# Optimization experiments

Measured on AMD Instinct MI355X. Metric: run time of the kernel, lower is better.

## Reference

```python
import jax, jax.numpy as jnp
import numpy as np

H = 16  # num_heads


def _rotate_half(t):
    d = t.shape[-1] // 2
    return jnp.concatenate((-t[..., d:], t[..., :d]), axis=-1)


def setup_inputs() -> dict:
    key = jax.random.key(0)
    ks = jax.random.split(key, 4)
    S, HID = 2048, 1280
    D = HID // H  # 80
    x = jax.random.normal(ks[0], (S, HID), dtype=jnp.float32)
    # rotary tables (seq_len, head_dim)
    inv_freq = 1.0 / (10000.0 ** (jnp.arange(0, D, 2, dtype=jnp.float32) / D))
    freqs = jnp.arange(S, dtype=jnp.float32)[:, None] * inv_freq[None, :]  # (S, D/2)
    emb = jnp.concatenate([freqs, freqs], axis=-1)  # (S, D)
    cos = jnp.cos(emb)
    sin = jnp.sin(emb)
    W_qkv = jax.random.normal(ks[1], (HID, 3 * HID), dtype=jnp.float32) * 0.02
    b_qkv = jnp.zeros((3 * HID,), dtype=jnp.float32)
    W_out = jax.random.normal(ks[2], (HID, HID), dtype=jnp.float32) * 0.02
    b_out = jnp.zeros((HID,), dtype=jnp.float32)
    # 8 windows of 256 tokens each -> block-diagonal attention
    cu_seqlens = jnp.arange(0, S + 1, 256, dtype=jnp.int32)  # (9,)
    return {"x": x, "cos": cos, "sin": sin, "W_qkv": W_qkv, "b_qkv": b_qkv,
            "W_out": W_out, "b_out": b_out, "cu_seqlens": cu_seqlens}


def _segment_mask(cu_seqlens, seq_len, dtype):
    positions = jnp.arange(seq_len)
    starts = cu_seqlens[:-1]
    ends = cu_seqlens[1:]
    in_segment = (positions[:, None] >= starts[None, :]) & (positions[:, None] < ends[None, :])
    segment_ids = jnp.argmax(in_segment.astype(jnp.int32), axis=-1)  # (S,)
    same_segment = segment_ids[:, None] == segment_ids[None, :]      # (S, S)
    return jnp.where(same_segment, jnp.zeros((), dtype), jnp.finfo(dtype).min)


def reference(x, cos, sin, W_qkv, b_qkv, W_out, b_out, cu_seqlens):
    S, HID = x.shape
    D = HID // H
    scale = D ** -0.5
    qkv = x @ W_qkv + b_qkv                       # (S, 3*HID)
    q, k, v = jnp.split(qkv, 3, axis=-1)
    q = q.reshape(S, H, D)
    k = k.reshape(S, H, D)
    v = v.reshape(S, H, D)
    cos_f = cos[:, :D][:, None, :]                # (S, 1, D)
    sin_f = sin[:, :D][:, None, :]
    q = q * cos_f + _rotate_half(q) * sin_f       # inline RoPE (fp32)
    k = k * cos_f + _rotate_half(k) * sin_f
    q = jnp.transpose(q, (1, 0, 2))               # (H, S, D)
    k = jnp.transpose(k, (1, 0, 2))
    v = jnp.transpose(v, (1, 0, 2))
    scores = jnp.einsum('hqd,hkd->hqk', q, k) * scale  # (H, S, S)
    mask = _segment_mask(cu_seqlens, S, scores.dtype)  # (S, S) block-diagonal bias
    scores = scores + mask[None, :, :]
    weights = jax.nn.softmax(scores, axis=-1)
    out = jnp.einsum('hqk,hkd->hqd', weights, v)       # (H, S, D)
    out = jnp.transpose(out, (1, 0, 2)).reshape(S, HID)
    return out @ W_out + b_out
```

## Files before the change

### kernel.cpp

```cpp
#include <hip/hip_runtime.h>


typedef short s16x8 __attribute__((ext_vector_type(8)));
typedef __bf16 bf16x8 __attribute__((ext_vector_type(8)));
typedef float f32x4 __attribute__((ext_vector_type(4)));
typedef unsigned short u16;
typedef unsigned long long u64;

__device__ __forceinline__ f32x4 mfma16(s16x8 a, s16x8 b, f32x4 c) {
  return __builtin_amdgcn_mfma_f32_16x16x32_bf16(
      __builtin_bit_cast(bf16x8, a), __builtin_bit_cast(bf16x8, b), c, 0, 0, 0);
}
__device__ __forceinline__ u16 f2b(float f) {
  union { float f; unsigned u; } v;
  v.f = f;
  unsigned r = v.u + 0x7fffu + ((v.u >> 16) & 1u);
  return (u16)(r >> 16);
}
__device__ __forceinline__ void gl16(const u16* g, u16* l) {
  __builtin_amdgcn_global_load_lds(
      (const __attribute__((address_space(1))) unsigned int*)(const void*)g,
      (__attribute__((address_space(3))) unsigned int*)(void*)l, 16, 0, 0);
}

__device__ __forceinline__ void transpose_body(const float* __restrict__ W,
                                               u16* __restrict__ WT, int K, int N,
                                               int nb, int kb, int t, float (*tile)[33]) {
  int tx = t & 31, ty = t >> 5;
#pragma unroll
  for (int r = 0; r < 32; r += 8)
    tile[ty + r][tx] = W[(long)(kb + ty + r) * N + nb + tx];
  __syncthreads();
#pragma unroll
  for (int r = 0; r < 32; r += 8)
    WT[(long)(nb + ty + r) * K + kb + tx] = f2b(tile[tx][ty + r]);
}

__global__ __launch_bounds__(256) void prep(const float* __restrict__ x,
                                            u16* __restrict__ xb,
                                            const float* __restrict__ Wqkv,
                                            u16* __restrict__ WqkvT,
                                            const float* __restrict__ Wout,
                                            u16* __restrict__ WoutT) {
  __shared__ float tile[32][33];
  int bid = blockIdx.x, t = threadIdx.x;
  if (bid < 2560) {
    int i = bid * 256 + t;
    float4 v = ((const float4*)x)[i];
    u64 pk = (u64)f2b(v.x) | ((u64)f2b(v.y) << 16) | ((u64)f2b(v.z) << 32) |
             ((u64)f2b(v.w) << 48);
    ((u64*)xb)[i] = pk;
  } else if (bid < 7360) {
    int i = bid - 2560;
    transpose_body(Wqkv, WqkvT, 1280, 3840, (i % 120) * 32, (i / 120) * 32, t, tile);
  } else {
    int i = bid - 7360;
    transpose_body(Wout, WoutT, 1280, 1280, (i % 40) * 32, (i / 40) * 32, t, tile);
  }
}

__global__ __launch_bounds__(256) void gemm_qkv_rope(const u16* __restrict__ A,
                                                     const u16* __restrict__ B,
                                                     const float* __restrict__ bias,
                                                     const float* __restrict__ cosb,
                                                     const float* __restrict__ sinb,
                                                     u16* __restrict__ Qr,
                                                     u16* __restrict__ Kr,
                                                     u16* __restrict__ VT) {
  __shared__ u16 As[64 * 32];
  __shared__ u16 Bs[160 * 32];
  const int K = 1280;
  int n0 = blockIdx.x * 160, m0 = blockIdx.y * 64;
  int t = threadIdx.x, w = t >> 6, lane = t & 63, lm = lane & 15, quad = lane >> 4;
  int wm = (w >> 1) * 32, wn = (w & 1) * 80;
  int srow = t >> 2;
  int scol = (((t & 3) ^ ((t >> 3) & 3))) * 8;
  const u16* Ag = A + (long)(m0 + srow) * K + scol;
  const u16* Bg = B + (long)(n0 + srow) * K + scol;
  const u16* Bg3 = B + (long)(n0 + 128 + srow) * K + scol;
  u16* AsW = As + w * 512;
  u16* BsW = Bs + w * 512;
  u16* BsW2 = Bs + 2048 + w * 512;
  u16* BsW3 = Bs + 4096 + w * 512;
  f32x4 acc[2][5] = {};
  for (int k0 = 0; k0 < K; k0 += 32) {
    __syncthreads();
    gl16(Ag + k0, AsW);
    gl16(Bg + k0, BsW);
    gl16(Bg + (long)64 * K + k0, BsW2);
    if (t < 128) gl16(Bg3 + k0, BsW3);
    __syncthreads();
    s16x8 af[2], bfr[5];
#pragma unroll
    for (int mt = 0; mt < 2; mt++) {
      int rm = wm + mt * 16 + lm;
      af[mt] = *(const s16x8*)&As[rm * 32 + ((quad ^ ((rm >> 1) & 3)) << 3)];
    }
#pragma unroll
    for (int nt = 0; nt < 5; nt++) {
      int rn = wn + nt * 16 + lm;
      bfr[nt] = *(const s16x8*)&Bs[rn * 32 + ((quad ^ ((rn >> 1) & 3)) << 3)];
    }
#pragma unroll
    for (int mt = 0; mt < 2; mt++)
#pragma unroll
      for (int nt = 0; nt < 5; nt++)
        acc[mt][nt] = mfma16(af[mt], bfr[nt], acc[mt][nt]);
  }

  int region = n0 / 1280;
  int hcol = (n0 - region * 1280 + wn) / 80;
  float bv[5];
#pragma unroll
  for (int nt = 0; nt < 5; nt++) bv[nt] = bias[n0 + wn + nt * 16 + lm];

  if (region == 2) {
#pragma unroll
    for (int mt = 0; mt < 2; mt++) {
      int sbase = m0 + wm + mt * 16 + quad * 4;
#pragma unroll
      for (int nt = 0; nt < 5; nt++) {
        int d = nt * 16 + lm;
        u64 pk = 0;
#pragma unroll
        for (int r = 0; r < 4; r++)
          pk |= (u64)f2b(acc[mt][nt][r] + bv[nt]) << (16 * r);
        *(u64*)&VT[((long)hcol * 80 + d) * 2048 + sbase] = pk;
      }
    }
    return;
  }

  const float scale = 0.111803398874989f;
  bool lo = lm < 8;
  u16* Out = (region == 0) ? Qr : Kr;
  float oscale = (region == 0) ? scale : 1.0f;
#pragma unroll
  for (int mt = 0; mt < 2; mt++)
#pragma unroll
    for (int r = 0; r < 4; r++) {
      int s = m0 + wm + mt * 16 + quad * 4 + r;
      float val[5], sw[5];
#pragma unroll
      for (int nt = 0; nt < 5; nt++) val[nt] = acc[mt][nt][r] + bv[nt];
#pragma unroll
      for (int nt = 0; nt < 5; nt++) sw[nt] = __shfl_xor(val[nt], 8);
      float rot[5];
      rot[0] = -(lo ? sw[2] : sw[3]);
      rot[1] = -(lo ? sw[3] : sw[4]);
      rot[2] = lo ? -sw[4] : sw[0];
      rot[3] = lo ? sw[0] : sw[1];
      rot[4] = lo ? sw[1] : sw[2];
      u16* orow = Out + ((long)hcol * 2048 + s) * 80;
      const float* crow = cosb + s * 80;
      const float* srw = sinb + s * 80;
#pragma unroll
      for (int nt = 0; nt < 5; nt++) {
        int d = nt * 16 + lm;
        orow[d] = f2b((val[nt] * crow[d] + rot[nt] * srw[d]) * oscale);
      }
    }
}

template <bool OUT_F32>
__global__ __launch_bounds__(256) void gemm_bt(const u16* __restrict__ A,
                                               const u16* __restrict__ B,
                                               const float* __restrict__ bias,
                                               void* __restrict__ Cout,
                                               int M, int N, int K) {
  __shared__ u16 As[64 * 32];
  __shared__ u16 Bs[128 * 32];
  int m0 = blockIdx.y * 64, n0 = blockIdx.x * 128;
  int t = threadIdx.x;
  int w = t >> 6, lane = t & 63, lm = lane & 15, quad = lane >> 4;
  int wm = (w >> 1) * 32, wn = (w & 1) * 64;
  int srow = t >> 2;
  int scol = (((t & 3) ^ ((t >> 3) & 3))) * 8;
  const u16* Ag = A + (long)(m0 + srow) * K + scol;
  const u16* Bg = B + (long)(n0 + srow) * K + scol;
  u16* AsW = As + w * 512;
  u16* BsW = Bs + w * 512;
  u16* BsW2 = Bs + 2048 + w * 512;
  f32x4 acc[2][4] = {};
  for (int k0 = 0; k0 < K; k0 += 32) {
    __syncthreads();
    gl16(Ag + k0, AsW);
    gl16(Bg + k0, BsW);
    gl16(Bg + (long)64 * K + k0, BsW2);
    __syncthreads();
    s16x8 af[2], bf[4];
#pragma unroll
    for (int mt = 0; mt < 2; mt++) {
      int rm = wm + mt * 16 + lm;
      af[mt] = *(const s16x8*)&As[rm * 32 + ((quad ^ ((rm >> 1) & 3)) << 3)];
    }
#pragma unroll
    for (int nt = 0; nt < 4; nt++) {
      int rn = wn + nt * 16 + lm;
      bf[nt] = *(const s16x8*)&Bs[rn * 32 + ((quad ^ ((rn >> 1) & 3)) << 3)];
    }
#pragma unroll
    for (int mt = 0; mt < 2; mt++)
#pragma unroll
      for (int nt = 0; nt < 4; nt++)
        acc[mt][nt] = mfma16(af[mt], bf[nt], acc[mt][nt]);
  }
#pragma unroll
  for (int mt = 0; mt < 2; mt++)
#pragma unroll
    for (int nt = 0; nt < 4; nt++) {
      int col = n0 + wn + nt * 16 + lm;
      float bvv = bias[col];
#pragma unroll
      for (int r = 0; r < 4; r++) {
        int row = m0 + wm + mt * 16 + quad * 4 + r;
        float v = acc[mt][nt][r] + bvv;
        if (OUT_F32) ((float*)Cout)[(long)row * N + col] = v;
        else ((u16*)Cout)[(long)row * N + col] = f2b(v);
      }
    }
}

__global__ __launch_bounds__(256, 1) void attn_kernel(const u16* __restrict__ Qr,
                                                      const u16* __restrict__ Kr,
                                                      const u16* __restrict__ VT,
                                                      u16* __restrict__ AO) {
  int qh = blockIdx.x, seg = blockIdx.y, h = blockIdx.z;
  int t = threadIdx.x;
  int w = t >> 6, lane = t & 63, lm = lane & 15, quad = lane >> 4;
  __shared__ u16 Ps[4][32 * 256];

  int s0 = seg * 256 + qh * 128 + w * 32;
  const u16* Qh = Qr + ((long)h * 2048 + s0) * 80;
  const u16* Kh = Kr + ((long)h * 2048 + seg * 256) * 80;

  f32x4 sc[2][16] = {};
  s16x8 zz = {};
#pragma unroll
  for (int kk = 0; kk < 3; kk++) {
    int dbase = kk * 32 + quad * 8;
    bool valid = dbase < 80;
    s16x8 af[2];
#pragma unroll
    for (int mt = 0; mt < 2; mt++)
      af[mt] = valid ? *(const s16x8*)(Qh + (mt * 16 + lm) * 80 + dbase) : zz;
#pragma unroll
    for (int nt = 0; nt < 16; nt++) {
      s16x8 bfr = valid ? *(const s16x8*)(Kh + (nt * 16 + lm) * 80 + dbase) : zz;
#pragma unroll
      for (int mt = 0; mt < 2; mt++)
        sc[mt][nt] = mfma16(af[mt], bfr, sc[mt][nt]);
    }
  }

  float rowinv[8];
#pragma unroll
  for (int mt = 0; mt < 2; mt++)
#pragma unroll
    for (int r = 0; r < 4; r++) {
      float m = sc[mt][0][r];
#pragma unroll
      for (int nt = 1; nt < 16; nt++) m = fmaxf(m, sc[mt][nt][r]);
      m = fmaxf(m, __shfl_xor(m, 1));
      m = fmaxf(m, __shfl_xor(m, 2));
      m = fmaxf(m, __shfl_xor(m, 4));
      m = fmaxf(m, __shfl_xor(m, 8));
      float s = 0.f;
#pragma unroll
      for (int nt = 0; nt < 16; nt++) {
        float e = __expf(sc[mt][nt][r] - m);
        sc[mt][nt][r] = e;
        s += e;
      }
      s += __shfl_xor(s, 1);
      s += __shfl_xor(s, 2);
      s += __shfl_xor(s, 4);
      s += __shfl_xor(s, 8);
      rowinv[mt * 4 + r] = 1.0f / s;
      int row = mt * 16 + quad * 4 + r;
#pragma unroll
      for (int nt = 0; nt < 16; nt++) {
        int chunk = nt * 2 + (lm >> 3);
        Ps[w][row * 256 + ((chunk ^ row) << 3) + (lm & 7)] = f2b(sc[mt][nt][r]);
      }
    }
  asm volatile("s_waitcnt lgkmcnt(0)" ::: "memory");

  f32x4 oacc[2][5] = {};
  const u16* Vh = VT + (long)h * 80 * 2048 + seg * 256;
#pragma unroll
  for (int kc = 0; kc < 8; kc++) {
    s16x8 pa[2];
#pragma unroll
    for (int mt = 0; mt < 2; mt++) {
      int row = mt * 16 + lm;
      pa[mt] = *(const s16x8*)&Ps[w][row * 256 + (((kc * 4 + quad) ^ row) << 3)];
    }
#pragma unroll
    for (int nt = 0; nt < 5; nt++) {
      s16x8 bvv = *(const s16x8*)(Vh + (long)(nt * 16 + lm) * 2048 + kc * 32 + quad * 8);
#pragma unroll
      for (int mt = 0; mt < 2; mt++)
        oacc[mt][nt] = mfma16(pa[mt], bvv, oacc[mt][nt]);
    }
  }
#pragma unroll
  for (int mt = 0; mt < 2; mt++)
#pragma unroll
    for (int nt = 0; nt < 5; nt++)
#pragma unroll
      for (int r = 0; r < 4; r++)
        AO[(long)(s0 + mt * 16 + quad * 4 + r) * 1280 + h * 80 + nt * 16 + lm] =
            f2b(oacc[mt][nt][r] * rowinv[mt * 4 + r]);
}

extern "C" void kernel_launch(void* const* d_in, const int* in_sizes, int n_in,
                              void* d_out, int out_size, void* d_ws, size_t ws_size,
                              hipStream_t stream) {
  const float* x    = (const float*)d_in[0];
  const float* cosb = (const float*)d_in[1];
  const float* sinb = (const float*)d_in[2];
  const float* Wqkv = (const float*)d_in[3];
  const float* bqkv = (const float*)d_in[4];
  const float* Wout = (const float*)d_in[5];
  const float* bout = (const float*)d_in[6];

  char* p = (char*)d_ws;
  u16* xb    = (u16*)p;
  u16* WqkvT = (u16*)(p + 5242880);
  u16* WoutT = (u16*)(p + 15073280);
  u16* Qr    = (u16*)(p + 18350080);
  u16* Kr    = (u16*)(p + 23592960);
  u16* VT    = (u16*)(p + 28835840);
  u16* AO    = xb;

  prep<<<dim3(8960), dim3(256), 0, stream>>>(x, xb, Wqkv, WqkvT, Wout, WoutT);
  gemm_qkv_rope<<<dim3(24, 32), dim3(256), 0, stream>>>(xb, WqkvT, bqkv, cosb, sinb,
                                                        Qr, Kr, VT);
  attn_kernel<<<dim3(2, 8, 16), dim3(256), 0, stream>>>(Qr, Kr, VT, AO);
  gemm_bt<true><<<dim3(10, 32), dim3(256), 0, stream>>>(AO, WoutT, bout, d_out,
                                                        2048, 1280, 1280);
}
```

Measured before the change: 173.6 us.

## Double the QKV GEMM K-tile and remap blocks for XCD-local reuse

The QKV+RoPE GEMM now stages a 64-wide K slice per iteration instead of 32, with a new XOR swizzle over eight 8-element chunks. This halves the number of barrier pairs per K loop and issues more loads per sync. Blocks are remapped from a 1D grid so that each XCD works on a fixed set of N-column tiles, which should improve L2 reuse of the weight matrix. The output GEMM grid is also transposed so that consecutive blocks share the same B tile. LDS use rises to about 28KB per block, which may reduce occupancy.

```diff
diff --git a/kernel.cpp b/kernel.cpp
--- a/kernel.cpp
+++ b/kernel.cpp
@@ -67,45 +67,54 @@
                                                      u16* __restrict__ Qr,
                                                      u16* __restrict__ Kr,
                                                      u16* __restrict__ VT) {
-  __shared__ u16 As[64 * 32];
-  __shared__ u16 Bs[160 * 32];
+  __shared__ u16 As[64 * 64];
+  __shared__ u16 Bs[160 * 64];
   const int K = 1280;
-  int n0 = blockIdx.x * 160, m0 = blockIdx.y * 64;
+  int i = blockIdx.x;
+  int xcd = i & 7, j = i >> 3;
+  int n0 = (xcd * 3 + (j % 3)) * 160;
+  int m0 = (j / 3) * 64;
   int t = threadIdx.x, w = t >> 6, lane = t & 63, lm = lane & 15, quad = lane >> 4;
   int wm = (w >> 1) * 32, wn = (w & 1) * 80;
-  int srow = t >> 2;
-  int scol = (((t & 3) ^ ((t >> 3) & 3))) * 8;
-  const u16* Ag = A + (long)(m0 + srow) * K + scol;
-  const u16* Bg = B + (long)(n0 + srow) * K + scol;
-  const u16* Bg3 = B + (long)(n0 + 128 + srow) * K + scol;
-  u16* AsW = As + w * 512;
-  u16* BsW = Bs + w * 512;
-  u16* BsW2 = Bs + 2048 + w * 512;
-  u16* BsW3 = Bs + 4096 + w * 512;
+  const u16* AgSrc[2];
+  const u16* BgSrc[5];
+#pragma unroll
+  for (int c = 0; c < 2; c++) {
+    int g = c * 256 + t, row = g >> 3, chp = g & 7;
+    AgSrc[c] = A + (long)(m0 + row) * K + ((chp ^ (row & 7)) << 3);
+  }
+#pragma unroll
+  for (int c = 0; c < 5; c++) {
+    int g = c * 256 + t, row = g >> 3, chp = g & 7;
+    BgSrc[c] = B + (long)(n0 + row) * K + ((chp ^ (row & 7)) << 3);
+  }
   f32x4 acc[2][5] = {};
-  for (int k0 = 0; k0 < K; k0 += 32) {
+  for (int k0 = 0; k0 < K; k0 += 64) {
     __syncthreads();
-    gl16(Ag + k0, AsW);
-    gl16(Bg + k0, BsW);
-    gl16(Bg + (long)64 * K + k0, BsW2);
-    if (t < 128) gl16(Bg3 + k0, BsW3);
+#pragma unroll
+    for (int c = 0; c < 2; c++) gl16(AgSrc[c] + k0, As + c * 2048 + w * 512);
+#pragma unroll
+    for (int c = 0; c < 5; c++) gl16(BgSrc[c] + k0, Bs + c * 2048 + w * 512);
     __syncthreads();
-    s16x8 af[2], bfr[5];
-#pragma unroll
-    for (int mt = 0; mt < 2; mt++) {
-      int rm = wm + mt * 16 + lm;
-      af[mt] = *(const s16x8*)&As[rm * 32 + ((quad ^ ((rm >> 1) & 3)) << 3)];
-    }
-#pragma unroll
-    for (int nt = 0; nt < 5; nt++) {
-      int rn = wn + nt * 16 + lm;
-      bfr[nt] = *(const s16x8*)&Bs[rn * 32 + ((quad ^ ((rn >> 1) & 3)) << 3)];
-    }
-#pragma unroll
-    for (int mt = 0; mt < 2; mt++)
-#pragma unroll
-      for (int nt = 0; nt < 5; nt++)
-        acc[mt][nt] = mfma16(af[mt], bfr[nt], acc[mt][nt]);
+#pragma unroll
+    for (int kh = 0; kh < 2; kh++) {
+      s16x8 af[2], bfr[5];
+#pragma unroll
+      for (int mt = 0; mt < 2; mt++) {
+        int rm = wm + mt * 16 + lm;
+        af[mt] = *(const s16x8*)&As[rm * 64 + (((kh * 4 + quad) ^ (rm & 7)) << 3)];
+      }
+#pragma unroll
+      for (int nt = 0; nt < 5; nt++) {
+        int rn = wn + nt * 16 + lm;
+        bfr[nt] = *(const s16x8*)&Bs[rn * 64 + (((kh * 4 + quad) ^ (rn & 7)) << 3)];
+      }
+#pragma unroll
+      for (int mt = 0; mt < 2; mt++)
+#pragma unroll
+        for (int nt = 0; nt < 5; nt++)
+          acc[mt][nt] = mfma16(af[mt], bfr[nt], acc[mt][nt]);
+    }
   }
 
   int region = n0 / 1280;
@@ -170,7 +179,7 @@
                                                int M, int N, int K) {
   __shared__ u16 As[64 * 32];
   __shared__ u16 Bs[128 * 32];
-  int m0 = blockIdx.y * 64, n0 = blockIdx.x * 128;
+  int m0 = blockIdx.x * 64, n0 = blockIdx.y * 128;
   int t = threadIdx.x;
   int w = t >> 6, lane = t & 63, lm = lane & 15, quad = lane >> 4;
   int wm = (w >> 1) * 32, wn = (w & 1) * 64;
@@ -335,9 +344,9 @@
   u16* AO    = xb;
 
   prep<<<dim3(8960), dim3(256), 0, stream>>>(x, xb, Wqkv, WqkvT, Wout, WoutT);
-  gemm_qkv_rope<<<dim3(24, 32), dim3(256), 0, stream>>>(xb, WqkvT, bqkv, cosb, sinb,
-                                                        Qr, Kr, VT);
+  gemm_qkv_rope<<<dim3(768), dim3(256), 0, stream>>>(xb, WqkvT, bqkv, cosb, sinb,
+                                                     Qr, Kr, VT);
   attn_kernel<<<dim3(2, 8, 16), dim3(256), 0, stream>>>(Qr, Kr, VT, AO);
-  gemm_bt<true><<<dim3(10, 32), dim3(256), 0, stream>>>(AO, WoutT, bout, d_out,
+  gemm_bt<true><<<dim3(32, 10), dim3(256), 0, stream>>>(AO, WoutT, bout, d_out,
                                                         2048, 1280, 1280);
 }
```

Result: faster. 164.9 us (-5.0%).
